# Optimization experiments

Measured on AMD Instinct MI355X. Metric: run time of the kernel, lower is better.

## Reference

```python
import jax, jax.numpy as jnp
import numpy as np

B = 2048          # number of trees (batch)
K = 511           # nodes per complete binary tree (depth 9: levels 0..8)
DEPTH = 9
VOCAB = 200000
EDIM = 128


def setup_inputs() -> dict:
    key = jax.random.key(0)
    k1, k2, k3, k4 = jax.random.split(key, 4)
    N = B * K
    i = np.arange(K)
    lvl = np.floor(np.log2(i + 1)).astype(np.int32)            # level within tree, 0..8
    par_local = np.where(i > 0, (i - 1) // 2, 0).astype(np.int64)  # root points to itself
    offs = (np.arange(B, dtype=np.int64) * K)[:, None]
    parent = jnp.asarray((offs + par_local[None, :]).reshape(-1), dtype=jnp.int32)
    level = jnp.asarray(np.tile(lvl, B), dtype=jnp.int32)
    batch_id = jnp.asarray(np.repeat(np.arange(B, dtype=np.int64), K), dtype=jnp.int32)
    tokens = jax.random.randint(k1, (N,), 0, VOCAB, dtype=jnp.int32)
    emb_weight = jax.random.normal(k2, (VOCAB, EDIM), dtype=jnp.float32) * 0.02
    W = jax.random.normal(k3, (EDIM, EDIM), dtype=jnp.float32) * 0.05
    b = jax.random.normal(k4, (EDIM,), dtype=jnp.float32) * 0.01
    return {"emb_weight": emb_weight, "W": W, "b": b,
            "tokens": tokens, "parent": parent, "level": level, "batch_id": batch_id}


def reference(emb_weight, W, b, tokens, parent, level, batch_id):
    # per-node projection: W_c(embedding(token))  -> [N, EDIM]
    h = emb_weight[tokens] @ W + b
    # bottom-up child aggregation: h[parent] += h[child], deepest level first
    for l in range(DEPTH - 1, 0, -1):
        contrib = jnp.where((level == l)[:, None], h, 0.0)
        h = h.at[parent].add(contrib)
    # torch.max over all node_list snapshots == per-tree elementwise max of node
    # states, clamped at 0 by the zero rows of untouched batch_node snapshots.
    seg_max = jax.ops.segment_max(h, batch_id, num_segments=B)
    return jnp.maximum(seg_max, 0.0)
```

## Files before the change

kernel.cpp:

```cpp
#include <hip/hip_runtime.h>
#include <hip/hip_bf16.h>
#include <stdint.h>

#define VOCAB 200000
#define EDIM 128
#define NTREES 2048
#define KNODES 511
#define PROJ_BLOCKS 512

typedef __attribute__((ext_vector_type(4))) float f32x4;
typedef __attribute__((ext_vector_type(2))) float f32x2;
typedef __attribute__((ext_vector_type(8))) short s16x8;
typedef __attribute__((ext_vector_type(8))) unsigned short u16x8;

__device__ __forceinline__ unsigned short f2bf(float x) {
  unsigned u = __builtin_bit_cast(unsigned, x);
  return (unsigned short)((u + 0x7fffu + ((u >> 16) & 1u)) >> 16);
}
__device__ __forceinline__ float bf2f(unsigned short h) {
  unsigned u = ((unsigned)h) << 16;
  return __builtin_bit_cast(float, u);
}

__device__ __forceinline__ unsigned fp8enc(float v) {
  unsigned u = __builtin_bit_cast(unsigned, v);
  unsigned s = (u >> 24) & 0x80u;
  unsigned au = u & 0x7fffffffu;
  au = au > 0x43E00000u ? 0x43E00000u : au;
  unsigned r = au + 0x0007ffffu + ((au >> 20) & 1u);
  unsigned code = (((r >> 23) - 120u) << 3) | ((r >> 20) & 7u);
  float a = __builtin_bit_cast(float, au);
  unsigned sub = (unsigned)(int)rintf(a * 512.0f);
  unsigned c = (au < 0x3C800000u) ? sub : code;
  return c | s;
}
__device__ __forceinline__ float fp8dec(unsigned b) {
  unsigned e = (b >> 3) & 15u, m = b & 7u;
  float n = __builtin_bit_cast(float, ((e + 120u) << 23) | (m << 20));
  float sv = (float)(int)m * 0.001953125f;
  float v = e ? n : sv;
  return (b & 0x80u) ? -v : v;
}

__device__ __forceinline__ unsigned enc4(float a, float b, float c, float d) {
#if __has_builtin(__builtin_amdgcn_cvt_pk_fp8_f32)
  int pk = 0;
  pk = __builtin_amdgcn_cvt_pk_fp8_f32(a, b, pk, false);
  pk = __builtin_amdgcn_cvt_pk_fp8_f32(c, d, pk, true);
  return (unsigned)pk;
#else
  return fp8enc(a) | (fp8enc(b) << 8) | (fp8enc(c) << 16) | (fp8enc(d) << 24);
#endif
}

__device__ __forceinline__ void dec8(uint2 v, float* o) {
#if __has_builtin(__builtin_amdgcn_cvt_pk_f32_fp8)
  f32x2 a = __builtin_amdgcn_cvt_pk_f32_fp8(v.x, false);
  f32x2 b = __builtin_amdgcn_cvt_pk_f32_fp8(v.x, true);
  f32x2 c = __builtin_amdgcn_cvt_pk_f32_fp8(v.y, false);
  f32x2 d = __builtin_amdgcn_cvt_pk_f32_fp8(v.y, true);
  o[0] = a[0]; o[1] = a[1]; o[2] = b[0]; o[3] = b[1];
  o[4] = c[0]; o[5] = c[1]; o[6] = d[0]; o[7] = d[1];
#else
#pragma unroll
  for (int i = 0; i < 4; ++i) o[i] = fp8dec((v.x >> (8 * i)) & 0xFFu);
#pragma unroll
  for (int i = 0; i < 4; ++i) o[4 + i] = fp8dec((v.y >> (8 * i)) & 0xFFu);
#endif
}

__device__ __forceinline__ s16x8 cvt8(f32x4 a, f32x4 b) {
  u16x8 t;
#pragma unroll
  for (int i = 0; i < 4; ++i)
    t[i] = __builtin_bit_cast(unsigned short, __float2bfloat16(a[i]));
#pragma unroll
  for (int i = 0; i < 4; ++i)
    t[4 + i] = __builtin_bit_cast(unsigned short, __float2bfloat16(b[i]));
  return __builtin_bit_cast(s16x8, t);
}

__global__ __launch_bounds__(256) void wprep_kernel(
    const float* __restrict__ W, const float* __restrict__ b,
    unsigned short* __restrict__ WTb, float* __restrict__ bsc) {
  int idx = blockIdx.x * 256 + threadIdx.x;
  if (idx < EDIM * EDIM) {
    int n = idx >> 7, k = idx & 127;
    WTb[idx] = f2bf(W[k * EDIM + n] * 64.0f);
  }
  if (idx < EDIM) bsc[idx] = b[idx] * 64.0f;
}

__global__ __launch_bounds__(256, 2) void proj_kernel(
    const float* __restrict__ emb, const unsigned short* __restrict__ WTb,
    const float* __restrict__ bsc, unsigned char* __restrict__ T8) {
  const int tid = threadIdx.x;
  const int w = tid >> 6, lane = tid & 63;
  const int q = lane >> 4, cl = lane & 15;

  s16x8 wf[4][8];
#pragma unroll
  for (int ks = 0; ks < 4; ++ks)
#pragma unroll
    for (int nt = 0; nt < 8; ++nt)
      wf[ks][nt] = *(const s16x8*)(WTb + (nt * 16 + cl) * EDIM + ks * 32 + q * 8);

  f32x4 bb[8];
#pragma unroll
  for (int nt = 0; nt < 8; ++nt) bb[nt] = *(const f32x4*)(bsc + nt * 16 + q * 4);

  const int NT = VOCAB / 64;
  for (int t = blockIdx.x; t < NT; t += PROJ_BLOCKS) {
    const long row = (long)t * 64 + w * 16 + cl;
    const float* rp = emb + row * EDIM + q * 8;

    f32x4 ea[4], eb[4];
#pragma unroll
    for (int ks = 0; ks < 4; ++ks) {
      ea[ks] = *(const f32x4*)(rp + ks * 32);
      eb[ks] = *(const f32x4*)(rp + ks * 32 + 4);
    }

    f32x4 acc[8];
#pragma unroll
    for (int nt = 0; nt < 8; ++nt) acc[nt] = bb[nt];

#pragma unroll
    for (int ks = 0; ks < 4; ++ks) {
      s16x8 ef = cvt8(ea[ks], eb[ks]);
#pragma unroll
      for (int nt = 0; nt < 8; ++nt)
        acc[nt] = __builtin_amdgcn_mfma_f32_16x16x32_bf16(wf[ks][nt], ef, acc[nt], 0, 0, 0);
    }

#pragma unroll
    for (int nt = 0; nt < 8; ++nt) {
      const int col0 = nt * 16 + q * 4;
      *(unsigned*)&T8[row * EDIM + col0] =
          enc4(acc[nt][0], acc[nt][1], acc[nt][2], acc[nt][3]);
    }
  }
}

__global__ __launch_bounds__(512, 4) void tree_kernel(
    const unsigned char* __restrict__ T8, const int* __restrict__ tokens,
    float* __restrict__ out) {
  __shared__ unsigned char P8[512][EDIM];
  unsigned char* lds = &P8[0][0];
  const int SOFF = 16384;
  const int MOFF = 53248;

  const int tid = threadIdx.x;
  const int tree = blockIdx.x;
  const int wv = tid >> 6, lane = tid & 63;

  const int* tk = tokens + (long)tree * KNODES;
  int toks[8];
#pragma unroll
  for (int i = 0; i < 8; ++i) {
    int node = wv * 64 + i * 8 + (lane >> 3);
    toks[i] = tk[node > 510 ? 510 : node];
  }
  const int chunk = (lane & 7) ^ ((lane >> 3) & 7);
#pragma unroll
  for (int i = 0; i < 8; ++i) {
    const unsigned char* src = T8 + (long)toks[i] * EDIM + chunk * 16;
    unsigned char* dst = &P8[wv * 64 + i * 8][0];
    __builtin_amdgcn_global_load_lds(
        (const __attribute__((address_space(1))) unsigned int*)src,
        (__attribute__((address_space(3))) unsigned int*)dst, 16, 0, 0);
  }
  __syncthreads();

  auto ldP8 = [&](int row, int q8) -> uint2 {
    int g = q8 >> 1, h = q8 & 1;
    return *(const uint2*)(lds + row * 128 + (((g ^ (row & 7))) << 4) + h * 8);
  };
  auto saddr = [&](int slot, int q16) -> unsigned char* {
    return lds + SOFF + slot * 288 + ((q16 ^ (slot & 7)) << 4);
  };

  const int q = tid & 15;
  const int jg = tid >> 4;
  float rmax[8];
#pragma unroll
  for (int e = 0; e < 8; ++e) rmax[e] = 0.f;

  u16x8 sp7[4];
#pragma unroll
  for (int k = 0; k < 4; ++k) {
    const int p = jg + 32 * k, m = 127 + p;
    uint2 pr = ldP8(m, q);
    uint2 xr = ldP8(2 * m + 1, q);
    uint2 yr = ldP8(2 * m + 2, q);
    float pv[8], xv[8], yv[8];
    dec8(pr, pv); dec8(xr, xv); dec8(yr, yv);
#pragma unroll
    for (int e = 0; e < 8; ++e) {
      float sv = pv[e] + xv[e] + yv[e];
      rmax[e] = fmaxf(rmax[e], fmaxf(fmaxf(xv[e], yv[e]), sv));
      sp7[k][e] = f2bf(sv);
    }
  }
  __syncthreads();
#pragma unroll
  for (int k = 0; k < 4; ++k) *(u16x8*)saddr(jg + 32 * k, q) = sp7[k];
  __syncthreads();

  for (int l = 6; l >= 0; --l) {
    const int cnt = 1 << l;
    for (int p = jg; p < cnt; p += 32) {
      const int m = cnt - 1 + p;
      const int ps = p << (7 - l);
      const int c2s = ps + (1 << (6 - l));
      uint2 pr = ldP8(m, q);
      u16x8 c1 = *(const u16x8*)saddr(ps, q);
      u16x8 c2 = *(const u16x8*)saddr(c2s, q);
      float pv[8];
      dec8(pr, pv);
      u16x8 sp;
#pragma unroll
      for (int e = 0; e < 8; ++e) {
        float sv = pv[e] + bf2f(c1[e]) + bf2f(c2[e]);
        rmax[e] = fmaxf(rmax[e], sv);
        sp[e] = f2bf(sv);
      }
      *(u16x8*)saddr(ps, q) = sp;
    }
    __syncthreads();
  }

#pragma unroll
  for (int e = 0; e < 8; ++e) {
    rmax[e] = fmaxf(rmax[e], __shfl_xor(rmax[e], 16, 64));
    rmax[e] = fmaxf(rmax[e], __shfl_xor(rmax[e], 32, 64));
  }
  float* mb = (float*)(lds + MOFF);
  if (lane < 16) {
#pragma unroll
    for (int e = 0; e < 8; ++e) mb[wv * 128 + lane * 8 + e] = rmax[e];
  }
  __syncthreads();
  if (tid < 128) {
    float v = mb[tid];
#pragma unroll
    for (int w2 = 1; w2 < 8; ++w2) v = fmaxf(v, mb[w2 * 128 + tid]);
    out[(long)tree * 128 + tid] = v * 0.015625f;
  }
}

extern "C" void kernel_launch(void* const* d_in, const int* in_sizes, int n_in,
                              void* d_out, int out_size, void* d_ws, size_t ws_size,
                              hipStream_t stream) {
  const float* emb = (const float*)d_in[0];
  const float* W = (const float*)d_in[1];
  const float* b = (const float*)d_in[2];
  const int* tokens = (const int*)d_in[3];

  unsigned char* T8 = (unsigned char*)d_ws;
  unsigned short* WTb = (unsigned short*)((char*)d_ws + 25600000);
  float* bsc = (float*)((char*)d_ws + 25632768);
  float* out = (float*)d_out;

  wprep_kernel<<<64, 256, 0, stream>>>(W, b, WTb, bsc);
  proj_kernel<<<PROJ_BLOCKS, 256, 0, stream>>>(emb, WTb, bsc, T8);
  tree_kernel<<<NTREES, 512, 0, stream>>>(T8, tokens, out);
}
```

Before: 76.16 us.

## Prefetch embedding tiles into LDS via async DMA in projection kernel

The projection kernel now loads each wave's next 16-row embedding tile into a swizzled LDS buffer with global_load_lds while the current tile's MFMAs run, replacing direct blocking global loads. The W fragments are pre-laid out by wprep in per-lane fragment order so each lane reads them with contiguous vector loads, and the launch changes to 256 blocks of 512 threads with per-wave 16-row tiles. The goal is to hide the latency of streaming the 100MB embedding table. The cost is single buffering with a full vmcnt wait, plus 64KB of LDS per block that may limit occupancy.

```diff
diff --git a/kernel.cpp b/kernel.cpp
--- a/kernel.cpp
+++ b/kernel.cpp
@@ -6,7 +6,6 @@
 #define EDIM 128
 #define NTREES 2048
 #define KNODES 511
-#define PROJ_BLOCKS 512
 
 typedef __attribute__((ext_vector_type(4))) float f32x4;
 typedef __attribute__((ext_vector_type(2))) float f32x2;
@@ -82,57 +81,95 @@
 
 __global__ __launch_bounds__(256) void wprep_kernel(
     const float* __restrict__ W, const float* __restrict__ b,
-    unsigned short* __restrict__ WTb, float* __restrict__ bsc) {
-  int idx = blockIdx.x * 256 + threadIdx.x;
-  if (idx < EDIM * EDIM) {
-    int n = idx >> 7, k = idx & 127;
-    WTb[idx] = f2bf(W[k * EDIM + n] * 64.0f);
-  }
-  if (idx < EDIM) bsc[idx] = b[idx] * 64.0f;
-}
-
-__global__ __launch_bounds__(256, 2) void proj_kernel(
-    const float* __restrict__ emb, const unsigned short* __restrict__ WTb,
+    unsigned short* __restrict__ WTb2, float* __restrict__ bsc) {
+  int c = blockIdx.x * 256 + threadIdx.x;
+  if (c < 2048) {
+    int lane = c & 63, fr = c >> 6;
+    int ks = fr >> 3, nt = fr & 7, q = lane >> 4, cl = lane & 15;
+    u16x8 t;
+#pragma unroll
+    for (int j = 0; j < 8; ++j)
+      t[j] = f2bf(W[(ks * 32 + q * 8 + j) * EDIM + nt * 16 + cl] * 64.0f);
+    *(u16x8*)(WTb2 + c * 8) = t;
+  }
+  if (c < EDIM) bsc[c] = b[c] * 64.0f;
+}
+
+__global__ __launch_bounds__(512, 2) void proj_kernel(
+    const float* __restrict__ emb, const unsigned short* __restrict__ WTb2,
     const float* __restrict__ bsc, unsigned char* __restrict__ T8) {
+  __shared__ float ES[8][16][EDIM];
+
   const int tid = threadIdx.x;
-  const int w = tid >> 6, lane = tid & 63;
+  const int wv = tid >> 6, lane = tid & 63;
   const int q = lane >> 4, cl = lane & 15;
 
-  s16x8 wf[4][8];
-#pragma unroll
-  for (int ks = 0; ks < 4; ++ks)
-#pragma unroll
-    for (int nt = 0; nt < 8; ++nt)
-      wf[ks][nt] = *(const s16x8*)(WTb + (nt * 16 + cl) * EDIM + ks * 32 + q * 8);
-
+  s16x8 wf[32];
+#pragma unroll
+  for (int fr = 0; fr < 32; ++fr)
+    wf[fr] = *(const s16x8*)(WTb2 + (fr * 64 + lane) * 8);
   f32x4 bb[8];
 #pragma unroll
-  for (int nt = 0; nt < 8; ++nt) bb[nt] = *(const f32x4*)(bsc + nt * 16 + q * 4);
-
-  const int NT = VOCAB / 64;
-  for (int t = blockIdx.x; t < NT; t += PROJ_BLOCKS) {
-    const long row = (long)t * 64 + w * 16 + cl;
-    const float* rp = emb + row * EDIM + q * 8;
+  for (int nt = 0; nt < 8; ++nt)
+    bb[nt] = *(const f32x4*)(bsc + nt * 16 + q * 4);
+#pragma unroll
+  for (int fr = 0; fr < 32; ++fr) asm volatile("" : "+v"(wf[fr]));
+#pragma unroll
+  for (int nt = 0; nt < 8; ++nt) asm volatile("" : "+v"(bb[nt]));
+
+  const int gw = blockIdx.x * 8 + wv;
+  const int NWT = VOCAB / 16;
+  const int STRIDE = 256 * 8;
+
+  auto issue_dma = [&](int t) {
+#pragma unroll
+    for (int i = 0; i < 8; ++i) {
+      int rloc = 2 * i + (lane >> 5);
+      int c5 = lane & 31;
+      int csrc = (c5 & 24) | ((c5 & 7) ^ (rloc & 7));
+      const float* src = emb + ((long)t * 16 + rloc) * EDIM + csrc * 4;
+      __builtin_amdgcn_global_load_lds(
+          (const __attribute__((address_space(1))) unsigned int*)src,
+          (__attribute__((address_space(3))) unsigned int*)(&ES[wv][2 * i][0]),
+          16, 0, 0);
+    }
+  };
+
+  int t = gw;
+  issue_dma(t);
+  for (; t < NWT; t += STRIDE) {
+    const int tn = t + STRIDE;
+
+    asm volatile("s_waitcnt vmcnt(0)" ::: "memory");
+    __builtin_amdgcn_sched_barrier(0);
 
     f32x4 ea[4], eb[4];
 #pragma unroll
     for (int ks = 0; ks < 4; ++ks) {
-      ea[ks] = *(const f32x4*)(rp + ks * 32);
-      eb[ks] = *(const f32x4*)(rp + ks * 32 + 4);
-    }
+      int g0 = ks * 8 + q * 2;
+      int s0 = (g0 & 24) | ((g0 & 7) ^ (cl & 7));
+      int g1 = g0 + 1;
+      int s1 = (g1 & 24) | ((g1 & 7) ^ (cl & 7));
+      const float* rb = &ES[wv][cl][0];
+      ea[ks] = *(const f32x4*)(rb + s0 * 4);
+      eb[ks] = *(const f32x4*)(rb + s1 * 4);
+    }
+    asm volatile("s_waitcnt lgkmcnt(0)" ::: "memory");
+    __builtin_amdgcn_sched_barrier(0);
+    if (tn < NWT) issue_dma(tn);
 
     f32x4 acc[8];
 #pragma unroll
     for (int nt = 0; nt < 8; ++nt) acc[nt] = bb[nt];
-
 #pragma unroll
     for (int ks = 0; ks < 4; ++ks) {
       s16x8 ef = cvt8(ea[ks], eb[ks]);
 #pragma unroll
       for (int nt = 0; nt < 8; ++nt)
-        acc[nt] = __builtin_amdgcn_mfma_f32_16x16x32_bf16(wf[ks][nt], ef, acc[nt], 0, 0, 0);
-    }
-
+        acc[nt] = __builtin_amdgcn_mfma_f32_16x16x32_bf16(wf[ks * 8 + nt], ef, acc[nt], 0, 0, 0);
+    }
+
+    const long row = (long)t * 16 + cl;
 #pragma unroll
     for (int nt = 0; nt < 8; ++nt) {
       const int col0 = nt * 16 + q * 4;
@@ -258,11 +295,11 @@
   const int* tokens = (const int*)d_in[3];
 
   unsigned char* T8 = (unsigned char*)d_ws;
-  unsigned short* WTb = (unsigned short*)((char*)d_ws + 25600000);
+  unsigned short* WTb2 = (unsigned short*)((char*)d_ws + 25600000);
   float* bsc = (float*)((char*)d_ws + 25632768);
   float* out = (float*)d_out;
 
-  wprep_kernel<<<64, 256, 0, stream>>>(W, b, WTb, bsc);
-  proj_kernel<<<PROJ_BLOCKS, 256, 0, stream>>>(emb, WTb, bsc, T8);
+  wprep_kernel<<<8, 256, 0, stream>>>(W, b, WTb2, bsc);
+  proj_kernel<<<256, 512, 0, stream>>>(emb, WTb2, bsc, T8);
   tree_kernel<<<NTREES, 512, 0, stream>>>(T8, tokens, out);
 }
```

New measurement: 66.38 us. -12.8%, faster.
